# Optimization experiments

Hardware: AMD Instinct MI355X
Metric: run time of the kernel (lower is better)

The kernel has to match this reference:

```python
import jax, jax.numpy as jnp
import numpy as np

N = 100000   # nodes
E = 1600000  # edges (avg degree 16)
D = 64       # in_dim == emb_dim
L = 3        # num_layers
G = 2000     # graphs in batch
LN_EPS = 1e-5


def setup_inputs() -> dict:
    key = jax.random.key(0)
    ks = jax.random.split(key, 14)
    s = 0.05  # xavier-ish small init scale
    x = jax.random.normal(ks[0], (N, D), jnp.float32)
    edge_index = jax.random.randint(ks[1], (2, E), 0, N, dtype=jnp.int32)
    batch = jnp.sort(jax.random.randint(ks[2], (N,), 0, G, dtype=jnp.int32))
    return {
        "x": x,
        "edge_index": edge_index,
        "batch": batch,
        # stacked per-layer GIN MLP params: Linear(D,D) -> SiLU -> Linear(D,D)
        "W1": jax.random.normal(ks[3], (L, D, D), jnp.float32) * s,
        "b1": jnp.zeros((L, D), jnp.float32),
        "W2": jax.random.normal(ks[4], (L, D, D), jnp.float32) * s,
        "b2": jnp.zeros((L, D), jnp.float32),
        "eps": jnp.zeros((L,), jnp.float32),  # trainable eps, init 0
        "ln_g": jnp.ones((L, D), jnp.float32),
        "ln_b": jnp.zeros((L, D), jnp.float32),
        # gate_nn: Linear(D, D//2) -> SiLU -> Linear(D//2, 1)
        "gw1": jax.random.normal(ks[5], (D, D // 2), jnp.float32) * s,
        "gb1": jnp.zeros((D // 2,), jnp.float32),
        "gw2": jax.random.normal(ks[6], (D // 2, 1), jnp.float32) * s,
        "gb2": jnp.zeros((1,), jnp.float32),
    }


def _layernorm(h, g, b):
    mu = jnp.mean(h, axis=-1, keepdims=True)
    var = jnp.mean(jnp.square(h - mu), axis=-1, keepdims=True)
    return (h - mu) * jax.lax.rsqrt(var + LN_EPS) * g + b


def reference(x, edge_index, batch, W1, b1, W2, b2, eps, ln_g, ln_b, gw1, gb1, gw2, gb2):
    src, dst = edge_index[0], edge_index[1]
    # ---- GIN layers (eval mode: dropout is identity) ----
    for l in range(L):
        agg = jax.ops.segment_sum(x[src], dst, num_segments=N)  # scatter-add of neighbor feats
        h = (1.0 + eps[l]) * x + agg                             # GIN update
        h = jax.nn.silu(h @ W1[l] + b1[l]) @ W2[l] + b2[l]       # 2-layer MLP
        x = _layernorm(h, ln_g[l], ln_b[l])
    # ---- GlobalAttention pooling ----
    gate = (jax.nn.silu(x @ gw1 + gb1) @ gw2 + gb2)[:, 0]        # [N]
    m = jax.ops.segment_max(gate, batch, num_segments=G)         # per-graph max for stability
    e = jnp.exp(gate - m[batch])
    denom = jax.ops.segment_sum(e, batch, num_segments=G)
    a = e / denom[batch]                                         # per-graph softmax
    out = jax.ops.segment_sum(a[:, None] * x, batch, num_segments=G)  # [G, D]
    return out
```

## Files before the change

### kernel.cpp

```cpp
#include <hip/hip_runtime.h>
#include <math.h>

#define NN 100000
#define NE 1600000
#define D 64
#define NG 2000
#define LN_EPS 1e-5f
#define NB ((NN + 255) / 256)
#define NBK NB
#define NTILE ((NN + 63) / 64)
#define EPB 6400

typedef __attribute__((ext_vector_type(8))) short short8;
typedef __attribute__((ext_vector_type(4))) float floatx4;

__device__ __forceinline__ unsigned short f2bf(float f) {
    unsigned int u = __float_as_uint(f);
    u += 0x7FFF + ((u >> 16) & 1);
    return (unsigned short)(u >> 16);
}
__device__ __forceinline__ float bfu2f(unsigned short v) {
    return __uint_as_float(((unsigned int)v) << 16);
}

__global__ __launch_bounds__(256) void k_conv(const float* __restrict__ x,
                                              unsigned short* __restrict__ xb) {
    int i = blockIdx.x * 256 + threadIdx.x;
    xb[i] = f2bf(x[i]);
}

__global__ __launch_bounds__(256) void k_bcount(const int* __restrict__ dst,
                                                int* __restrict__ btot) {
    __shared__ int lcnt[NBK];
    int e0 = blockIdx.x * EPB;
    int tid = threadIdx.x;
    for (int i = tid; i < NBK; i += 256) lcnt[i] = 0;
    __syncthreads();
    for (int k = 0; k < EPB; k += 256)
        atomicAdd(&lcnt[dst[e0 + k + tid] >> 8], 1);
    __syncthreads();
    for (int i = tid; i < NBK; i += 256) {
        int c = lcnt[i];
        if (c) atomicAdd(&btot[i], c);
    }
}

__global__ __launch_bounds__(512) void k_bscan(const int* __restrict__ btot,
                                               int* __restrict__ bbase) {
    __shared__ int s[512];
    int t = threadIdx.x;
    int v = (t < NB) ? btot[t] : 0;
    s[t] = v;
    __syncthreads();
    for (int off = 1; off < 512; off <<= 1) {
        int u = (t >= off) ? s[t - off] : 0;
        __syncthreads();
        s[t] += u;
        __syncthreads();
    }
    if (t < NB) bbase[t] = s[t] - v;
    if (t == NB - 1) bbase[NB] = s[t];
}

__global__ __launch_bounds__(512) void k_bcurinit(const int* __restrict__ bbase,
                                                  int* __restrict__ bcur,
                                                  int* __restrict__ row_ptr) {
    int b = threadIdx.x;
    if (b < NBK) bcur[b * 16] = bbase[b];
    if (b == 0) row_ptr[NN] = NE;
}

__global__ __launch_bounds__(256) void k_part(const int* __restrict__ src,
                                              const int* __restrict__ dst,
                                              int* __restrict__ bcur,
                                              unsigned int* __restrict__ tmp) {
    __shared__ int lcnt[NBK];
    __shared__ int lbase[NBK];
    __shared__ int sd[EPB];
    __shared__ int ss[EPB];
    int e0 = blockIdx.x * EPB;
    int tid = threadIdx.x;

    for (int i = tid; i < NBK; i += 256) lcnt[i] = 0;
    __syncthreads();

    for (int k = 0; k < EPB; k += 256) {
        int d = dst[e0 + k + tid];
        int s = src[e0 + k + tid];
        sd[k + tid] = d;
        ss[k + tid] = s;
        atomicAdd(&lcnt[d >> 8], 1);
    }
    __syncthreads();

    for (int i = tid; i < NBK; i += 256) {
        int c = lcnt[i];
        lbase[i] = c ? atomicAdd(&bcur[i * 16], c) : 0;
        lcnt[i] = 0;
    }
    __syncthreads();

    for (int k = 0; k < EPB; k += 256) {
        int d = sd[k + tid];
        int s = ss[k + tid];
        int b = d >> 8;
        int pos = lbase[b] + atomicAdd(&lcnt[b], 1);
        tmp[pos] = ((unsigned int)s << 8) | (unsigned int)(d & 255);
    }
}

__global__ __launch_bounds__(256) void k_bfill(const unsigned int* __restrict__ tmp,
                                               const int* __restrict__ bbase,
                                               int* __restrict__ row_ptr,
                                               int* __restrict__ col) {
    __shared__ int lcur[256];
    __shared__ int wsum[4];
    int b = blockIdx.x;
    int nb0 = b * 256;
    int nodes = min(256, NN - nb0);
    int tid = threadIdx.x;
    int lane = tid & 63;
    int w = tid >> 6;
    int estart = bbase[b], eend = bbase[b + 1];

    lcur[tid] = 0;
    __syncthreads();
    for (int e = estart + tid; e < eend; e += 256)
        atomicAdd(&lcur[tmp[e] & 255], 1);
    __syncthreads();

    int v = lcur[tid];
    int x = v;
#pragma unroll
    for (int off = 1; off < 64; off <<= 1) {
        int u = __shfl_up(x, off, 64);
        if (lane >= off) x += u;
    }
    if (lane == 63) wsum[w] = x;
    __syncthreads();
    int base = estart;
    for (int k = 0; k < w; k++) base += wsum[k];
    int rp = base + x - v;
    if (tid < nodes) row_ptr[nb0 + tid] = rp;
    lcur[tid] = rp;
    __syncthreads();

    for (int e = estart + tid; e < eend; e += 256) {
        unsigned int p = tmp[e];
        int pos = atomicAdd(&lcur[p & 255], 1);
        col[pos] = (int)(p >> 8);
    }
}

__global__ __launch_bounds__(256) void k_gather(const unsigned short* __restrict__ xin,
                                                unsigned short* __restrict__ h,
                                                const int* __restrict__ row_ptr,
                                                const int* __restrict__ col,
                                                const float* __restrict__ epsp) {
    int w = threadIdx.x >> 6;
    int lane = threadIdx.x & 63;
    int g = lane >> 4;
    int fl = lane & 15;
    int node = (blockIdx.x * 4 + w) * 4 + g;
    int start = row_ptr[node], end = row_ptr[node + 1];

    float4 A0 = {0, 0, 0, 0}, A1 = {0, 0, 0, 0}, A2 = {0, 0, 0, 0}, A3 = {0, 0, 0, 0};
    for (int eb = start; eb < end; eb += 16) {
        int cnt = min(16, end - eb);
        int c = (fl < cnt) ? col[eb + fl] : 0;
        int j = 0;
        for (; j + 4 <= cnt; j += 4) {
            int i0 = __shfl(c, g * 16 + j, 64);
            int i1 = __shfl(c, g * 16 + j + 1, 64);
            int i2 = __shfl(c, g * 16 + j + 2, 64);
            int i3 = __shfl(c, g * 16 + j + 3, 64);
            ushort4 v0 = *(const ushort4*)(xin + ((size_t)i0 << 6) + fl * 4);
            ushort4 v1 = *(const ushort4*)(xin + ((size_t)i1 << 6) + fl * 4);
            ushort4 v2 = *(const ushort4*)(xin + ((size_t)i2 << 6) + fl * 4);
            ushort4 v3 = *(const ushort4*)(xin + ((size_t)i3 << 6) + fl * 4);
            A0.x += bfu2f(v0.x); A0.y += bfu2f(v0.y); A0.z += bfu2f(v0.z); A0.w += bfu2f(v0.w);
            A1.x += bfu2f(v1.x); A1.y += bfu2f(v1.y); A1.z += bfu2f(v1.z); A1.w += bfu2f(v1.w);
            A2.x += bfu2f(v2.x); A2.y += bfu2f(v2.y); A2.z += bfu2f(v2.z); A2.w += bfu2f(v2.w);
            A3.x += bfu2f(v3.x); A3.y += bfu2f(v3.y); A3.z += bfu2f(v3.z); A3.w += bfu2f(v3.w);
        }
        for (; j < cnt; j++) {
            int i0 = __shfl(c, g * 16 + j, 64);
            ushort4 v0 = *(const ushort4*)(xin + ((size_t)i0 << 6) + fl * 4);
            A0.x += bfu2f(v0.x); A0.y += bfu2f(v0.y); A0.z += bfu2f(v0.z); A0.w += bfu2f(v0.w);
        }
    }
    float ev = 1.0f + *epsp;
    ushort4 xs = *(const ushort4*)(xin + ((size_t)node << 6) + fl * 4);
    ushort4 o;
    o.x = f2bf(ev * bfu2f(xs.x) + ((A0.x + A1.x) + (A2.x + A3.x)));
    o.y = f2bf(ev * bfu2f(xs.y) + ((A0.y + A1.y) + (A2.y + A3.y)));
    o.z = f2bf(ev * bfu2f(xs.z) + ((A0.z + A1.z) + (A2.z + A3.z)));
    o.w = f2bf(ev * bfu2f(xs.w) + ((A0.w + A1.w) + (A2.w + A3.w)));
    *(ushort4*)(h + ((size_t)node << 6) + fl * 4) = o;
}

template <int LAST>
__global__ __launch_bounds__(256) void k_mfma(const unsigned short* __restrict__ h,
                                              unsigned short* __restrict__ xout,
                                              const float* __restrict__ W1,
                                              const float* __restrict__ b1,
                                              const float* __restrict__ W2,
                                              const float* __restrict__ b2,
                                              const float* __restrict__ lng,
                                              const float* __restrict__ lnb,
                                              const float* __restrict__ gw1,
                                              const float* __restrict__ gb1,
                                              const float* __restrict__ gw2,
                                              const float* __restrict__ gb2,
                                              float* __restrict__ gate) {
    __shared__ unsigned short a2[4][16 * 64];
    int w = threadIdx.x >> 6;
    int lane = threadIdx.x & 63;
    int n = lane & 15;
    int q = lane >> 4;
    int base = blockIdx.x * 64 + w * 16;

    short8 B1f[2][4], B2f[2][4];
#pragma unroll
    for (int ks = 0; ks < 2; ks++)
#pragma unroll
        for (int c = 0; c < 4; c++) {
            short8 f1, f2;
#pragma unroll
            for (int j = 0; j < 8; j++) {
                int k = ks * 32 + q * 8 + j;
                f1[j] = (short)f2bf(W1[k * 64 + c * 16 + n]);
                f2[j] = (short)f2bf(W2[k * 64 + c * 16 + n]);
            }
            B1f[ks][c] = f1;
            B2f[ks][c] = f2;
        }

    float b1v[4], b2v[4], lgv[4], lbv[4];
#pragma unroll
    for (int c = 0; c < 4; c++) {
        b1v[c] = b1[c * 16 + n];
        b2v[c] = b2[c * 16 + n];
        lgv[c] = lng[c * 16 + n];
        lbv[c] = lnb[c * 16 + n];
    }

    int mnode = base + n;
    int mc = min(mnode, NN - 1);
    const short8* hp = (const short8*)(h + ((size_t)mc << 6));
    short8 A0 = hp[q];
    short8 A1 = hp[4 + q];

    floatx4 acc1[4];
#pragma unroll
    for (int c = 0; c < 4; c++) {
        floatx4 a = {b1v[c], b1v[c], b1v[c], b1v[c]};
        a = __builtin_amdgcn_mfma_f32_16x16x32_bf16(A0, B1f[0][c], a, 0, 0, 0);
        a = __builtin_amdgcn_mfma_f32_16x16x32_bf16(A1, B1f[1][c], a, 0, 0, 0);
        acc1[c] = a;
    }

    unsigned short* aw = a2[w];
#pragma unroll
    for (int c = 0; c < 4; c++)
#pragma unroll
        for (int r = 0; r < 4; r++) {
            float v = acc1[c][r];
            v = v / (1.0f + __expf(-v));
            aw[(q * 4 + r) * 64 + c * 16 + n] = f2bf(v);
        }

    const short8* ap = (const short8*)(aw + n * 64);
    short8 A20 = ap[q];
    short8 A21 = ap[4 + q];

    floatx4 acc2[4];
#pragma unroll
    for (int c = 0; c < 4; c++) {
        floatx4 a = {b2v[c], b2v[c], b2v[c], b2v[c]};
        a = __builtin_amdgcn_mfma_f32_16x16x32_bf16(A20, B2f[0][c], a, 0, 0, 0);
        a = __builtin_amdgcn_mfma_f32_16x16x32_bf16(A21, B2f[1][c], a, 0, 0, 0);
        acc2[c] = a;
    }

    float mu[4], inv[4];
#pragma unroll
    for (int r = 0; r < 4; r++) {
        float s = acc2[0][r] + acc2[1][r] + acc2[2][r] + acc2[3][r];
#pragma unroll
        for (int off = 1; off < 16; off <<= 1) s += __shfl_xor(s, off, 64);
        mu[r] = s * (1.0f / 64.0f);
        float d0 = acc2[0][r] - mu[r], d1 = acc2[1][r] - mu[r];
        float d2 = acc2[2][r] - mu[r], d3 = acc2[3][r] - mu[r];
        float vv = d0 * d0 + d1 * d1 + d2 * d2 + d3 * d3;
#pragma unroll
        for (int off = 1; off < 16; off <<= 1) vv += __shfl_xor(vv, off, 64);
        inv[r] = rsqrtf(vv * (1.0f / 64.0f) + LN_EPS);
    }

#pragma unroll
    for (int c = 0; c < 4; c++)
#pragma unroll
        for (int r = 0; r < 4; r++) {
            int node = base + q * 4 + r;
            float o = (acc2[c][r] - mu[r]) * inv[r] * lgv[c] + lbv[c];
            unsigned short ob = f2bf(o);
            if (node < NN) xout[((size_t)node << 6) + c * 16 + n] = ob;
            if (LAST) aw[(q * 4 + r) * 64 + c * 16 + n] = ob;
        }

    if (LAST) {
        short8 B3f[2][2];
#pragma unroll
        for (int ks = 0; ks < 2; ks++)
#pragma unroll
            for (int c = 0; c < 2; c++) {
                short8 f;
#pragma unroll
                for (int j = 0; j < 8; j++) {
                    int k = ks * 32 + q * 8 + j;
                    f[j] = (short)f2bf(gw1[k * 32 + c * 16 + n]);
                }
                B3f[ks][c] = f;
            }
        const short8* gp = (const short8*)(aw + n * 64);
        short8 G0 = gp[q];
        short8 G1 = gp[4 + q];
        floatx4 acc3[2];
#pragma unroll
        for (int c = 0; c < 2; c++) {
            float bv = gb1[c * 16 + n];
            floatx4 a = {bv, bv, bv, bv};
            a = __builtin_amdgcn_mfma_f32_16x16x32_bf16(G0, B3f[0][c], a, 0, 0, 0);
            a = __builtin_amdgcn_mfma_f32_16x16x32_bf16(G1, B3f[1][c], a, 0, 0, 0);
            acc3[c] = a;
        }
        float gw2v0 = gw2[n], gw2v1 = gw2[16 + n];
        float gb2v = gb2[0];
#pragma unroll
        for (int r = 0; r < 4; r++) {
            float v0 = acc3[0][r];
            v0 = v0 / (1.0f + __expf(-v0));
            float v1 = acc3[1][r];
            v1 = v1 / (1.0f + __expf(-v1));
            float gsum = v0 * gw2v0 + v1 * gw2v1;
#pragma unroll
            for (int off = 1; off < 16; off <<= 1) gsum += __shfl_xor(gsum, off, 64);
            int node = base + q * 4 + r;
            if (n == 0 && node < NN) gate[node] = gsum + gb2v;
        }
    }
}

__global__ __launch_bounds__(256) void k_pool(const unsigned short* __restrict__ xf,
                                              const float* __restrict__ gate,
                                              const int* __restrict__ batch,
                                              float* __restrict__ out) {
    __shared__ float redm[4];
    __shared__ float reds[4];
    __shared__ float racc[4][D];
    int g = blockIdx.x;
    int w = threadIdx.x >> 6;
    int lane = threadIdx.x & 63;

    int lo = 0, hi = NN;
    while (lo < hi) { int mid = (lo + hi) >> 1; if (batch[mid] < g) lo = mid + 1; else hi = mid; }
    int start = lo;
    hi = NN;
    while (lo < hi) { int mid = (lo + hi) >> 1; if (batch[mid] < g + 1) lo = mid + 1; else hi = mid; }
    int end = lo;

    if (start >= end) {
        if (w == 0) out[((size_t)g << 6) + lane] = 0.0f;
        return;
    }

    float m = -INFINITY;
    for (int i = start + (int)threadIdx.x; i < end; i += 256) m = fmaxf(m, gate[i]);
#pragma unroll
    for (int mm = 32; mm >= 1; mm >>= 1) m = fmaxf(m, __shfl_xor(m, mm, 64));
    if (lane == 0) redm[w] = m;
    __syncthreads();
    m = fmaxf(fmaxf(redm[0], redm[1]), fmaxf(redm[2], redm[3]));

    float s = 0.0f;
    for (int i = start + (int)threadIdx.x; i < end; i += 256) s += __expf(gate[i] - m);
#pragma unroll
    for (int mm = 32; mm >= 1; mm >>= 1) s += __shfl_xor(s, mm, 64);
    if (lane == 0) reds[w] = s;
    __syncthreads();
    s = (reds[0] + reds[1]) + (reds[2] + reds[3]);

    float acc = 0.0f;
    for (int i = start + w; i < end; i += 4)
        acc += __expf(gate[i] - m) * bfu2f(xf[((size_t)i << 6) + lane]);
    racc[w][lane] = acc;
    __syncthreads();
    if (w == 0)
        out[((size_t)g << 6) + lane] =
            ((racc[0][lane] + racc[1][lane]) + (racc[2][lane] + racc[3][lane])) / s;
}

extern "C" void kernel_launch(void* const* d_in, const int* in_sizes, int n_in,
                              void* d_out, int out_size, void* d_ws, size_t ws_size,
                              hipStream_t stream) {
    const float* x   = (const float*)d_in[0];
    const int* ei    = (const int*)d_in[1];
    const int* batch = (const int*)d_in[2];
    const float* W1  = (const float*)d_in[3];
    const float* b1  = (const float*)d_in[4];
    const float* W2  = (const float*)d_in[5];
    const float* b2  = (const float*)d_in[6];
    const float* eps = (const float*)d_in[7];
    const float* lng = (const float*)d_in[8];
    const float* lnb = (const float*)d_in[9];
    const float* gw1 = (const float*)d_in[10];
    const float* gb1 = (const float*)d_in[11];
    const float* gw2 = (const float*)d_in[12];
    const float* gb2 = (const float*)d_in[13];

    const int* src = ei;
    const int* dst = ei + NE;

    unsigned short* xb = (unsigned short*)d_ws;
    unsigned short* h  = xb + (size_t)NN * D;
    float* gate        = (float*)(h + (size_t)NN * D);
    int* row_ptr       = (int*)(gate + NN);
    int* col           = row_ptr + NN + 1;
    unsigned int* tmp  = (unsigned int*)(col + NE);
    int* btot          = (int*)(tmp + NE);
    int* bbase         = btot + NB;
    int* bcur          = bbase + NB + 1;

    float* out = (float*)d_out;

    hipMemsetAsync(btot, 0, (size_t)NB * sizeof(int), stream);
    k_conv<<<(NN * D) / 256, 256, 0, stream>>>(x, xb);
    k_bcount<<<NE / EPB, 256, 0, stream>>>(dst, btot);
    k_bscan<<<1, 512, 0, stream>>>(btot, bbase);
    k_bcurinit<<<1, 512, 0, stream>>>(bbase, bcur, row_ptr);
    k_part<<<NE / EPB, 256, 0, stream>>>(src, dst, bcur, tmp);
    k_bfill<<<NBK, 256, 0, stream>>>(tmp, bbase, row_ptr, col);

    k_gather<<<NN / 16, 256, 0, stream>>>(xb, h, row_ptr, col, eps + 0);
    k_mfma<0><<<NTILE, 256, 0, stream>>>(h, xb,
        W1 + 0 * D * D, b1 + 0 * D, W2 + 0 * D * D, b2 + 0 * D,
        lng + 0 * D, lnb + 0 * D, gw1, gb1, gw2, gb2, gate);

    k_gather<<<NN / 16, 256, 0, stream>>>(xb, h, row_ptr, col, eps + 1);
    k_mfma<0><<<NTILE, 256, 0, stream>>>(h, xb,
        W1 + 1 * D * D, b1 + 1 * D, W2 + 1 * D * D, b2 + 1 * D,
        lng + 1 * D, lnb + 1 * D, gw1, gb1, gw2, gb2, gate);

    k_gather<<<NN / 16, 256, 0, stream>>>(xb, h, row_ptr, col, eps + 2);
    k_mfma<1><<<NTILE, 256, 0, stream>>>(h, xb,
        W1 + 2 * D * D, b1 + 2 * D, W2 + 2 * D * D, b2 + 2 * D,
        lng + 2 * D, lnb + 2 * D, gw1, gb1, gw2, gb2, gate);

    k_pool<<<NG, 256, 0, stream>>>(xb, gate, batch, out);
}
```

Measured before the change: 341.3 us.

## Prepack bf16 weight fragments once and process multiple tiles per MLP block

Adds a prep kernel that converts W1/W2/gw1 to bf16 and lays them out in MFMA fragment order, so each MLP block loads its B fragments with vector loads instead of converting them element by element. The MLP kernel now loops over three 64-node tiles per block, which spreads the weight-load cost over more nodes. LDS row stride is padded to 72 to reduce bank conflicts. This adds one extra launch and gives fewer blocks, which lowers parallelism per launch.

Result: no change. 343.9 us (+0.8%).

```diff
diff --git a/kernel.cpp b/kernel.cpp
--- a/kernel.cpp
+++ b/kernel.cpp
@@ -10,6 +10,11 @@
 #define NBK NB
 #define NTILE ((NN + 63) / 64)
 #define EPB 6400
+#define TPB 3
+#define NMB ((NTILE + TPB - 1) / TPB)
+#define LSTR 72
+#define WFRAG_MLP 24576
+#define WFRAG_TOT 26624
 
 typedef __attribute__((ext_vector_type(8))) short short8;
 typedef __attribute__((ext_vector_type(4))) float floatx4;
@@ -27,6 +32,37 @@
                                               unsigned short* __restrict__ xb) {
     int i = blockIdx.x * 256 + threadIdx.x;
     xb[i] = f2bf(x[i]);
+}
+
+__global__ __launch_bounds__(256) void k_wprep(const float* __restrict__ W1,
+                                               const float* __restrict__ W2,
+                                               const float* __restrict__ gw1,
+                                               unsigned short* __restrict__ wfrag) {
+    int idx = blockIdx.x * 256 + threadIdx.x;
+    if (idx < WFRAG_MLP) {
+        int l = idx / 8192;
+        int rem = idx % 8192;
+        int mat = rem / 4096;
+        int r2 = rem % 4096;
+        int ks = r2 / 2048;
+        int c = (r2 / 512) % 4;
+        int lane = (r2 / 8) % 64;
+        int j = r2 % 8;
+        int n = lane & 15, q = lane >> 4;
+        int k = ks * 32 + q * 8 + j;
+        int col = c * 16 + n;
+        const float* Wm = mat ? W2 : W1;
+        wfrag[idx] = f2bf(Wm[l * 4096 + k * 64 + col]);
+    } else if (idx < WFRAG_TOT) {
+        int g = idx - WFRAG_MLP;
+        int ks = g / 1024;
+        int c = (g / 512) % 2;
+        int lane = (g / 8) % 64;
+        int j = g % 8;
+        int n = lane & 15, q = lane >> 4;
+        int k = ks * 32 + q * 8 + j;
+        wfrag[idx] = f2bf(gw1[k * 32 + c * 16 + n]);
+    }
 }
 
 __global__ __launch_bounds__(256) void k_bcount(const int* __restrict__ dst,
@@ -202,39 +238,38 @@
 template <int LAST>
 __global__ __launch_bounds__(256) void k_mfma(const unsigned short* __restrict__ h,
                                               unsigned short* __restrict__ xout,
-                                              const float* __restrict__ W1,
+                                              const short8* __restrict__ wf,
+                                              const short8* __restrict__ gf,
                                               const float* __restrict__ b1,
-                                              const float* __restrict__ W2,
                                               const float* __restrict__ b2,
                                               const float* __restrict__ lng,
                                               const float* __restrict__ lnb,
-                                              const float* __restrict__ gw1,
                                               const float* __restrict__ gb1,
                                               const float* __restrict__ gw2,
                                               const float* __restrict__ gb2,
                                               float* __restrict__ gate) {
-    __shared__ unsigned short a2[4][16 * 64];
+    __shared__ __align__(16) unsigned short a2[4][16 * LSTR];
     int w = threadIdx.x >> 6;
     int lane = threadIdx.x & 63;
     int n = lane & 15;
     int q = lane >> 4;
-    int base = blockIdx.x * 64 + w * 16;
 
     short8 B1f[2][4], B2f[2][4];
 #pragma unroll
     for (int ks = 0; ks < 2; ks++)
 #pragma unroll
         for (int c = 0; c < 4; c++) {
-            short8 f1, f2;
-#pragma unroll
-            for (int j = 0; j < 8; j++) {
-                int k = ks * 32 + q * 8 + j;
-                f1[j] = (short)f2bf(W1[k * 64 + c * 16 + n]);
-                f2[j] = (short)f2bf(W2[k * 64 + c * 16 + n]);
-            }
-            B1f[ks][c] = f1;
-            B2f[ks][c] = f2;
-        }
+            B1f[ks][c] = wf[(ks * 4 + c) * 64 + lane];
+            B2f[ks][c] = wf[512 + (ks * 4 + c) * 64 + lane];
+        }
+    short8 B3f[2][2];
+    if (LAST) {
+#pragma unroll
+        for (int ks = 0; ks < 2; ks++)
+#pragma unroll
+            for (int c = 0; c < 2; c++)
+                B3f[ks][c] = gf[(ks * 2 + c) * 64 + lane];
+    }
 
     float b1v[4], b2v[4], lgv[4], lbv[4];
 #pragma unroll
@@ -244,110 +279,107 @@
         lgv[c] = lng[c * 16 + n];
         lbv[c] = lnb[c * 16 + n];
     }
-
-    int mnode = base + n;
-    int mc = min(mnode, NN - 1);
-    const short8* hp = (const short8*)(h + ((size_t)mc << 6));
-    short8 A0 = hp[q];
-    short8 A1 = hp[4 + q];
-
-    floatx4 acc1[4];
-#pragma unroll
-    for (int c = 0; c < 4; c++) {
-        floatx4 a = {b1v[c], b1v[c], b1v[c], b1v[c]};
-        a = __builtin_amdgcn_mfma_f32_16x16x32_bf16(A0, B1f[0][c], a, 0, 0, 0);
-        a = __builtin_amdgcn_mfma_f32_16x16x32_bf16(A1, B1f[1][c], a, 0, 0, 0);
-        acc1[c] = a;
+    float gb1v[2], gw2v[2], gb2v = 0.f;
+    if (LAST) {
+        gb1v[0] = gb1[n]; gb1v[1] = gb1[16 + n];
+        gw2v[0] = gw2[n]; gw2v[1] = gw2[16 + n];
+        gb2v = gb2[0];
     }
 
     unsigned short* aw = a2[w];
-#pragma unroll
-    for (int c = 0; c < 4; c++)
+
+    for (int t = 0; t < TPB; t++) {
+        int tile = blockIdx.x * TPB + t;
+        if (tile >= NTILE) break;
+        int base = tile * 64 + w * 16;
+
+        int mnode = base + n;
+        int mc = min(mnode, NN - 1);
+        const short8* hp = (const short8*)(h + ((size_t)mc << 6));
+        short8 A0 = hp[q];
+        short8 A1 = hp[4 + q];
+
+        floatx4 acc1[4];
+#pragma unroll
+        for (int c = 0; c < 4; c++) {
+            floatx4 a = {b1v[c], b1v[c], b1v[c], b1v[c]};
+            a = __builtin_amdgcn_mfma_f32_16x16x32_bf16(A0, B1f[0][c], a, 0, 0, 0);
+            a = __builtin_amdgcn_mfma_f32_16x16x32_bf16(A1, B1f[1][c], a, 0, 0, 0);
+            acc1[c] = a;
+        }
+
+#pragma unroll
+        for (int c = 0; c < 4; c++)
+#pragma unroll
+            for (int r = 0; r < 4; r++) {
+                float v = acc1[c][r];
+                v = v / (1.0f + __expf(-v));
+                aw[(q * 4 + r) * LSTR + c * 16 + n] = f2bf(v);
+            }
+
+        const short8* ap = (const short8*)(aw + n * LSTR);
+        short8 A20 = ap[q];
+        short8 A21 = ap[4 + q];
+
+        floatx4 acc2[4];
+#pragma unroll
+        for (int c = 0; c < 4; c++) {
+            floatx4 a = {b2v[c], b2v[c], b2v[c], b2v[c]};
+            a = __builtin_amdgcn_mfma_f32_16x16x32_bf16(A20, B2f[0][c], a, 0, 0, 0);
+            a = __builtin_amdgcn_mfma_f32_16x16x32_bf16(A21, B2f[1][c], a, 0, 0, 0);
+            acc2[c] = a;
+        }
+
+        float mu[4], inv[4];
 #pragma unroll
         for (int r = 0; r < 4; r++) {
-            float v = acc1[c][r];
-            v = v / (1.0f + __expf(-v));
-            aw[(q * 4 + r) * 64 + c * 16 + n] = f2bf(v);
-        }
-
-    const short8* ap = (const short8*)(aw + n * 64);
-    short8 A20 = ap[q];
-    short8 A21 = ap[4 + q];
-
-    floatx4 acc2[4];
-#pragma unroll
-    for (int c = 0; c < 4; c++) {
-        floatx4 a = {b2v[c], b2v[c], b2v[c], b2v[c]};
-        a = __builtin_amdgcn_mfma_f32_16x16x32_bf16(A20, B2f[0][c], a, 0, 0, 0);
-        a = __builtin_amdgcn_mfma_f32_16x16x32_bf16(A21, B2f[1][c], a, 0, 0, 0);
-        acc2[c] = a;
-    }
-
-    float mu[4], inv[4];
-#pragma unroll
-    for (int r = 0; r < 4; r++) {
-        float s = acc2[0][r] + acc2[1][r] + acc2[2][r] + acc2[3][r];
-#pragma unroll
-        for (int off = 1; off < 16; off <<= 1) s += __shfl_xor(s, off, 64);
-        mu[r] = s * (1.0f / 64.0f);
-        float d0 = acc2[0][r] - mu[r], d1 = acc2[1][r] - mu[r];
-        float d2 = acc2[2][r] - mu[r], d3 = acc2[3][r] - mu[r];
-        float vv = d0 * d0 + d1 * d1 + d2 * d2 + d3 * d3;
-#pragma unroll
-        for (int off = 1; off < 16; off <<= 1) vv += __shfl_xor(vv, off, 64);
-        inv[r] = rsqrtf(vv * (1.0f / 64.0f) + LN_EPS);
-    }
-
-#pragma unroll
-    for (int c = 0; c < 4; c++)
-#pragma unroll
-        for (int r = 0; r < 4; r++) {
-            int node = base + q * 4 + r;
-            float o = (acc2[c][r] - mu[r]) * inv[r] * lgv[c] + lbv[c];
-            unsigned short ob = f2bf(o);
-            if (node < NN) xout[((size_t)node << 6) + c * 16 + n] = ob;
-            if (LAST) aw[(q * 4 + r) * 64 + c * 16 + n] = ob;
-        }
-
-    if (LAST) {
-        short8 B3f[2][2];
-#pragma unroll
-        for (int ks = 0; ks < 2; ks++)
+            float s = acc2[0][r] + acc2[1][r] + acc2[2][r] + acc2[3][r];
+#pragma unroll
+            for (int off = 1; off < 16; off <<= 1) s += __shfl_xor(s, off, 64);
+            mu[r] = s * (1.0f / 64.0f);
+            float d0 = acc2[0][r] - mu[r], d1 = acc2[1][r] - mu[r];
+            float d2 = acc2[2][r] - mu[r], d3 = acc2[3][r] - mu[r];
+            float vv = d0 * d0 + d1 * d1 + d2 * d2 + d3 * d3;
+#pragma unroll
+            for (int off = 1; off < 16; off <<= 1) vv += __shfl_xor(vv, off, 64);
+            inv[r] = rsqrtf(vv * (1.0f / 64.0f) + LN_EPS);
+        }
+
+#pragma unroll
+        for (int c = 0; c < 4; c++)
+#pragma unroll
+            for (int r = 0; r < 4; r++) {
+                int node = base + q * 4 + r;
+                float o = (acc2[c][r] - mu[r]) * inv[r] * lgv[c] + lbv[c];
+                unsigned short ob = f2bf(o);
+                if (node < NN) xout[((size_t)node << 6) + c * 16 + n] = ob;
+                if (LAST) aw[(q * 4 + r) * LSTR + c * 16 + n] = ob;
+            }
+
+        if (LAST) {
+            const short8* gp = (const short8*)(aw + n * LSTR);
+            short8 G0 = gp[q];
+            short8 G1 = gp[4 + q];
+            floatx4 acc3[2];
 #pragma unroll
             for (int c = 0; c < 2; c++) {
-                short8 f;
-#pragma unroll
-                for (int j = 0; j < 8; j++) {
-                    int k = ks * 32 + q * 8 + j;
-                    f[j] = (short)f2bf(gw1[k * 32 + c * 16 + n]);
-                }
-                B3f[ks][c] = f;
+                floatx4 a = {gb1v[c], gb1v[c], gb1v[c], gb1v[c]};
+                a = __builtin_amdgcn_mfma_f32_16x16x32_bf16(G0, B3f[0][c], a, 0, 0, 0);
+                a = __builtin_amdgcn_mfma_f32_16x16x32_bf16(G1, B3f[1][c], a, 0, 0, 0);
+                acc3[c] = a;
             }
-        const short8* gp = (const short8*)(aw + n * 64);
-        short8 G0 = gp[q];
-        short8 G1 = gp[4 + q];
-        floatx4 acc3[2];
-#pragma unroll
-        for (int c = 0; c < 2; c++) {
-            float bv = gb1[c * 16 + n];
-            floatx4 a = {bv, bv, bv, bv};
-            a = __builtin_amdgcn_mfma_f32_16x16x32_bf16(G0, B3f[0][c], a, 0, 0, 0);
-            a = __builtin_amdgcn_mfma_f32_16x16x32_bf16(G1, B3f[1][c], a, 0, 0, 0);
-            acc3[c] = a;
-        }
-        float gw2v0 = gw2[n], gw2v1 = gw2[16 + n];
-        float gb2v = gb2[0];
-#pragma unroll
-        for (int r = 0; r < 4; r++) {
-            float v0 = acc3[0][r];
-            v0 = v0 / (1.0f + __expf(-v0));
-            float v1 = acc3[1][r];
-            v1 = v1 / (1.0f + __expf(-v1));
-            float gsum = v0 * gw2v0 + v1 * gw2v1;
-#pragma unroll
-            for (int off = 1; off < 16; off <<= 1) gsum += __shfl_xor(gsum, off, 64);
-            int node = base + q * 4 + r;
-            if (n == 0 && node < NN) gate[node] = gsum + gb2v;
+#pragma unroll
+            for (int r = 0; r < 4; r++) {
+                float v0 = acc3[0][r];
+                v0 = v0 / (1.0f + __expf(-v0));
+                float v1 = acc3[1][r];
+                v1 = v1 / (1.0f + __expf(-v1));
+                float gsum = v0 * gw2v[0] + v1 * gw2v[1];
+#pragma unroll
+                for (int off = 1; off < 16; off <<= 1) gsum += __shfl_xor(gsum, off, 64);
+                int node = base + q * 4 + r;
+                if (n == 0 && node < NN) gate[node] = gsum + gb2v;
+            }
         }
     }
 }
@@ -422,40 +454,44 @@
     const int* src = ei;
     const int* dst = ei + NE;
 
-    unsigned short* xb = (unsigned short*)d_ws;
-    unsigned short* h  = xb + (size_t)NN * D;
-    float* gate        = (float*)(h + (size_t)NN * D);
-    int* row_ptr       = (int*)(gate + NN);
-    int* col           = row_ptr + NN + 1;
-    unsigned int* tmp  = (unsigned int*)(col + NE);
-    int* btot          = (int*)(tmp + NE);
-    int* bbase         = btot + NB;
-    int* bcur          = bbase + NB + 1;
+    unsigned short* xb    = (unsigned short*)d_ws;
+    unsigned short* h     = xb + (size_t)NN * D;
+    float* gate           = (float*)(h + (size_t)NN * D);
+    int* row_ptr          = (int*)(gate + NN);
+    int* col              = row_ptr + NN + 1;
+    unsigned int* tmp     = (unsigned int*)(col + NE);
+    int* btot             = (int*)(tmp + NE);
+    int* bbase            = btot + NB;
+    int* bcur             = bbase + NB + 1;
+    unsigned short* wfrag = (unsigned short*)(bcur + NBK * 16);
 
     float* out = (float*)d_out;
 
     hipMemsetAsync(btot, 0, (size_t)NB * sizeof(int), stream);
     k_conv<<<(NN * D) / 256, 256, 0, stream>>>(x, xb);
+    k_wprep<<<WFRAG_TOT / 256, 256, 0, stream>>>(W1, W2, gw1, wfrag);
     k_bcount<<<NE / EPB, 256, 0, stream>>>(dst, btot);
     k_bscan<<<1, 512, 0, stream>>>(btot, bbase);
     k_bcurinit<<<1, 512, 0, stream>>>(bbase, bcur, row_ptr);
     k_part<<<NE / EPB, 256, 0, stream>>>(src, dst, bcur, tmp);
     k_bfill<<<NBK, 256, 0, stream>>>(tmp, bbase, row_ptr, col);
 
+    const short8* wf0 = (const short8*)(wfrag);
+    const short8* wf1 = (const short8*)(wfrag + 8192);
+    const short8* wf2 = (const short8*)(wfrag + 16384);
+    const short8* gf  = (const short8*)(wfrag + WFRAG_MLP);
+
     k_gather<<<NN / 16, 256, 0, stream>>>(xb, h, row_ptr, col, eps + 0);
-    k_mfma<0><<<NTILE, 256, 0, stream>>>(h, xb,
-        W1 + 0 * D * D, b1 + 0 * D, W2 + 0 * D * D, b2 + 0 * D,
-        lng + 0 * D, lnb + 0 * D, gw1, gb1, gw2, gb2, gate);
+    k_mfma<0><<<NMB, 256, 0, stream>>>(h, xb, wf0, gf,
+        b1 + 0 * D, b2 + 0 * D, lng + 0 * D, lnb + 0 * D, gb1, gw2, gb2, gate);
 
     k_gather<<<NN / 16, 256, 0, stream>>>(xb, h, row_ptr, col, eps + 1);
-    k_mfma<0><<<NTILE, 256, 0, stream>>>(h, xb,
-        W1 + 1 * D * D, b1 + 1 * D, W2 + 1 * D * D, b2 + 1 * D,
-        lng + 1 * D, lnb + 1 * D, gw1, gb1, gw2, gb2, gate);
+    k_mfma<0><<<NMB, 256, 0, stream>>>(h, xb, wf1, gf,
+        b1 + 1 * D, b2 + 1 * D, lng + 1 * D, lnb + 1 * D, gb1, gw2, gb2, gate);
 
     k_gather<<<NN / 16, 256, 0, stream>>>(xb, h, row_ptr, col, eps + 2);
-    k_mfma<1><<<NTILE, 256, 0, stream>>>(h, xb,
-        W1 + 2 * D * D, b1 + 2 * D, W2 + 2 * D * D, b2 + 2 * D,
-        lng + 2 * D, lnb + 2 * D, gw1, gb1, gw2, gb2, gate);
+    k_mfma<1><<<NMB, 256, 0, stream>>>(h, xb, wf2, gf,
+        b1 + 2 * D, b2 + 2 * D, lng + 2 * D, lnb + 2 * D, gb1, gw2, gb2, gate);
 
     k_pool<<<NG, 256, 0, stream>>>(xb, gate, batch, out);
 }
```
